# Kernel optimization log

Hardware: AMD Instinct MI355X
Metric: run time of the kernel (lower is better)

Reference implementation:

```python
import jax, jax.numpy as jnp
import numpy as np

B, INPUTS, HIDDEN, OUTPUTS = 128, 512, 512, 512
MAXLEN = INPUTS  # required by the module's bmm/cat shape constraints


def setup_inputs() -> dict:
    key = jax.random.key(0)
    ks = jax.random.split(key, 11)
    s = 0.03
    return {
        "x": jax.random.normal(ks[0], (B, INPUTS, MAXLEN), jnp.float32),
        "attn_W": jax.random.normal(ks[1], (MAXLEN, HIDDEN + INPUTS), jnp.float32) * s,
        "attn_b": jax.random.normal(ks[2], (MAXLEN,), jnp.float32) * s,
        "comb_W": jax.random.normal(ks[3], (HIDDEN, INPUTS + MAXLEN), jnp.float32) * s,
        "comb_b": jax.random.normal(ks[4], (HIDDEN,), jnp.float32) * s,
        "w_ih": jax.random.normal(ks[5], (3 * HIDDEN, HIDDEN), jnp.float32) * s,
        "w_hh": jax.random.normal(ks[6], (3 * HIDDEN, HIDDEN), jnp.float32) * s,
        "b_ih": jax.random.normal(ks[7], (3 * HIDDEN,), jnp.float32) * s,
        "b_hh": jax.random.normal(ks[8], (3 * HIDDEN,), jnp.float32) * s,
        "out_W": jax.random.normal(ks[9], (OUTPUTS, HIDDEN), jnp.float32) * s,
        "out_b": jax.random.normal(ks[10], (OUTPUTS,), jnp.float32) * s,
    }


def reference(x, attn_W, attn_b, comb_W, comb_b, w_ih, w_hh, b_ih, b_hh, out_W, out_b):
    # x: [B, inputs, T] with T == max_length == inputs (shape constraint of the module).
    # The torch code loops over batch with identical per-element math -> vectorize over B,
    # and uses lax.scan over the sequential time dimension.
    Bn = x.shape[0]
    H = w_hh.shape[1]
    xs = jnp.moveaxis(x, 2, 0)  # [T, B, inputs]
    h0 = jnp.zeros((Bn, H), x.dtype)

    def step(h, inp):
        # inp: [B, inputs], h: [B, hidden]
        cat = jnp.concatenate([inp, h], axis=1)                     # [B, inputs+hidden]
        attn_w = jax.nn.softmax(cat @ attn_W.T + attn_b, axis=1)    # [B, max_length]
        applied = jnp.einsum('bm,bmt->bt', attn_w, x)               # [B, T]
        g = jnp.concatenate([inp, applied], axis=1) @ comb_W.T + comb_b
        g = jax.nn.relu(g)                                          # [B, hidden]
        # PyTorch GRU cell
        gi = g @ w_ih.T + b_ih
        gh = h @ w_hh.T + b_hh
        ir, iz, i_n = jnp.split(gi, 3, axis=1)
        hr, hz, h_n = jnp.split(gh, 3, axis=1)
        r = jax.nn.sigmoid(ir + hr)
        z = jax.nn.sigmoid(iz + hz)
        n = jnp.tanh(i_n + r * h_n)
        h_new = (1.0 - z) * n + z * h
        return h_new, None

    h_final, _ = jax.lax.scan(step, h0, xs)
    return h_final @ out_W.T + out_b  # [B, outputs]
```

## Files before the change

kernel.cpp:

```cpp
#include <hip/hip_runtime.h>


typedef unsigned short u16;
typedef unsigned int u32;
typedef _Float16 h2 __attribute__((ext_vector_type(2)));
typedef _Float16 f16x8 __attribute__((ext_vector_type(8)));
typedef float f32x4 __attribute__((ext_vector_type(4)));
typedef float f32x2 __attribute__((ext_vector_type(2)));
typedef u32 u32x4 __attribute__((ext_vector_type(4)));

#define MAGIC 0x13579BDFu

#define OFF_AW   65536
#define OFF_CW   1114112
#define OFF_WIH  2162688
#define OFF_WHH  3735552
#define OFF_OW   5308416
#define OFF_HB   5832704
#define OFF_SF   5963776
#define OFF_AP0  6225920
#define OFF_AP1  6488064
#define OFF_GB   6750208
#define OFF_GH   6881280
#define OFF_XT   7667712
#define WS_NEED  74776576

#define FS_S   64
#define FS_C   96
#define FS_G   128
#define FS_GH  160
#define FS_H   192
#define FS_RDY 224

__device__ __forceinline__ float sigmoidf_(float v) { return 1.f / (1.f + __expf(-v)); }
__device__ __forceinline__ float tanhf_(float v) {
  v = fminf(fmaxf(v, -15.f), 15.f);
  float e2 = __expf(2.f * v);
  return (e2 - 1.f) / (e2 + 1.f);
}
__device__ __forceinline__ u32 packh2(float a, float b) {
  h2 v; v.x = (_Float16)a; v.y = (_Float16)b;
  return __builtin_bit_cast(u32, v);
}

__device__ __forceinline__ void vm_drain() { asm volatile("s_waitcnt vmcnt(0)" ::: "memory"); }

__device__ __forceinline__ f32x2 ldg_f32x2(const void* p) {
  f32x2 r;
  asm volatile("global_load_dwordx2 %0, %1, off sc0 sc1\n\ts_waitcnt vmcnt(0)"
               : "=v"(r) : "v"(p) : "memory");
  return r;
}
__device__ __forceinline__ void ldg4x16(const void* p0, const void* p1, const void* p2,
                                        const void* p3, u32x4& a, u32x4& b, u32x4& c, u32x4& d) {
  asm volatile(
      "global_load_dwordx4 %0, %4, off sc0 sc1\n\t"
      "global_load_dwordx4 %1, %5, off sc0 sc1\n\t"
      "global_load_dwordx4 %2, %6, off sc0 sc1\n\t"
      "global_load_dwordx4 %3, %7, off sc0 sc1\n\t"
      "s_waitcnt vmcnt(0)"
      : "=&v"(a), "=&v"(b), "=&v"(c), "=&v"(d)
      : "v"(p0), "v"(p1), "v"(p2), "v"(p3) : "memory");
}
__device__ __forceinline__ void ldg3_f32(const float* p0, const float* p1, const float* p2,
                                         float& a, float& b, float& c) {
  asm volatile(
      "global_load_dword %0, %3, off sc0 sc1\n\t"
      "global_load_dword %1, %4, off sc0 sc1\n\t"
      "global_load_dword %2, %5, off sc0 sc1\n\t"
      "s_waitcnt vmcnt(0)"
      : "=&v"(a), "=&v"(b), "=&v"(c)
      : "v"(p0), "v"(p1), "v"(p2) : "memory");
}

__device__ __forceinline__ void stg_f32(float* p, float v) {
  asm volatile("global_store_dword %0, %1, off sc0 sc1" :: "v"(p), "v"(v) : "memory");
}
__device__ __forceinline__ void stg_f32x2(float* p, f32x2 v) {
  asm volatile("global_store_dwordx2 %0, %1, off sc0 sc1" :: "v"(p), "v"(v) : "memory");
}
__device__ __forceinline__ void stg_u16(u16* p, u32 v) {
  asm volatile("global_store_short %0, %1, off sc0 sc1" :: "v"(p), "v"(v) : "memory");
}

__device__ __forceinline__ void flag_arrive(u32* ctrl, int fs, int slot, u32 tok) {
  vm_drain();
  __syncthreads();
  if (threadIdx.x == 0) {
    atomicMax(ctrl + fs + slot, tok);
  }
}
__device__ __forceinline__ void flag_wait(u32* ctrl, int fs, int n, u32 tok, int lane) {
  if (tok == 0u) return;
  u32* p = ctrl + fs;
  for (;;) {
    u32 v = tok;
    if (lane < n) v = __hip_atomic_load(p + lane, __ATOMIC_RELAXED, __HIP_MEMORY_SCOPE_AGENT);
    if (__all((int)(v >= tok))) break;
  }
}

__device__ __forceinline__ void stage_rows(const u16* gsrc, char* lds, int tid) {
  const int row = tid >> 4, c = tid & 15;
  const u16* g = gsrc + row * 512 + c * 32;
  u32x4 a, b, cc, d;
  ldg4x16(g, g + 8, g + 16, g + 24, a, b, cc, d);
  u32x4* dst = (u32x4*)(lds + row * 1040 + c * 64);
  dst[0] = a; dst[1] = b; dst[2] = cc; dst[3] = d;
}

#define MFMA(a, b, c) __builtin_amdgcn_mfma_f32_16x16x32_f16((a), (b), (c), 0, 0, 0)

extern "C" __global__ void __launch_bounds__(256, 1)
rnn_fused(const float* __restrict__ x, const float* __restrict__ attn_W,
          const float* __restrict__ attn_b, const float* __restrict__ comb_W,
          const float* __restrict__ comb_b, const float* __restrict__ w_ih,
          const float* __restrict__ w_hh, const float* __restrict__ b_ih,
          const float* __restrict__ b_hh, const float* __restrict__ out_W,
          const float* __restrict__ out_b, float* __restrict__ out,
          char* __restrict__ ws)
{
  const int tid  = threadIdx.x;
  const int lane = tid & 63;
  const int warp = tid >> 6;
  const int team = blockIdx.x & 7;
  const int tb   = blockIdx.x >> 3;
  const int tt   = tb * 256 + tid;
  const int gb0  = team * 16;
  const int lb   = tb >> 1;
  const int half = tb & 1;
  const int b    = gb0 + lb;
  const int m0h  = half * 256;

  u32* ctrl = (u32*)ws + team * 1024;

  u16*   AW  = (u16*)(ws + OFF_AW);
  u16*   CW  = (u16*)(ws + OFF_CW);
  u16*   WIH = (u16*)(ws + OFF_WIH);
  u16*   WHH = (u16*)(ws + OFF_WHH);
  u16*   OW  = (u16*)(ws + OFF_OW);
  u16*   HB  = (u16*)(ws + OFF_HB);
  float* Sf  = (float*)(ws + OFF_SF);
  float* AP0 = (float*)(ws + OFF_AP0);
  float* AP1 = (float*)(ws + OFF_AP1);
  u16*   GB  = (u16*)(ws + OFF_GB);
  float* GH  = (float*)(ws + OFF_GH);
  u16*   XT  = (u16*)(ws + OFF_XT);

  __shared__ char smem[16704];
  float*     tbuf   = (float*)smem;
  u32*       pLDS   = (u32*)smem;
  float*     redbuf = (float*)(smem + 512);
  float*     rbuf   = (float*)(smem + 8704);
  _Float16*  ldsF   = (_Float16*)smem;

  if (tb == 0) {
    for (int i = 1 + tid; i < 1024; i += 256) ctrl[i] = 0u;
    __syncthreads();
    if (tid == 0) { __threadfence(); atomicExch(ctrl, MAGIC); }
  }
  if (tid == 0) {
    while (__hip_atomic_load(ctrl, __ATOMIC_RELAXED, __HIP_MEMORY_SCOPE_AGENT) != MAGIC) {}
    __threadfence();
  }
  __syncthreads();

  for (int i = tt; i < 512 * 1024; i += 8192) AW[i]  = __builtin_bit_cast(u16, (_Float16)attn_W[i]);
  for (int i = tt; i < 512 * 1024; i += 8192) CW[i]  = __builtin_bit_cast(u16, (_Float16)comb_W[i]);
  for (int i = tt; i < 1536 * 512; i += 8192) WIH[i] = __builtin_bit_cast(u16, (_Float16)w_ih[i]);
  for (int i = tt; i < 1536 * 512; i += 8192) WHH[i] = __builtin_bit_cast(u16, (_Float16)w_hh[i]);
  for (int i = tt; i < 512 * 512;  i += 8192) OW[i]  = __builtin_bit_cast(u16, (_Float16)out_W[i]);
  HB[(size_t)gb0 * 512 + tt] = 0;

  {
    const float* xb  = x  + (size_t)b * 512 * 512;
    u16*         xtB = XT + (size_t)b * 512 * 512;
    for (int mt = 0; mt < 4; ++mt) {
      for (int ct = 0; ct < 8; ++ct) {
        for (int rr = warp; rr < 64; rr += 4)
          tbuf[rr * 65 + lane] = xb[(size_t)(m0h + mt * 64 + rr) * 512 + ct * 64 + lane];
        __syncthreads();
        for (int rr = warp; rr < 64; rr += 4)
          xtB[(size_t)(ct * 64 + rr) * 512 + m0h + mt * 64 + lane] =
              __builtin_bit_cast(u16, (_Float16)tbuf[lane * 65 + rr]);
        __syncthreads();
      }
    }
  }

  vm_drain();
  __syncthreads();
  if (tid == 0) { __threadfence(); atomicMax(ctrl + FS_RDY + tb, 1u); }
  {
    u32* p = ctrl + FS_RDY;
    for (;;) {
      u32 v = 1u;
      if (lane < 32) v = __hip_atomic_load(p + lane, __ATOMIC_RELAXED, __HIP_MEMORY_SCOPE_AGENT);
      if (__all((int)(v >= 1u))) break;
    }
  }
  __syncthreads();
  __threadfence();

  uint4 xr4[64];
  {
    const u16* base = XT + (size_t)b * 262144 + m0h + warp * 64;
#pragma unroll
    for (int r = 0; r < 8; ++r) {
      const uint4* row = (const uint4*)(base + (size_t)(lane * 8 + r) * 512);
#pragma unroll
      for (int jj = 0; jj < 8; ++jj) xr4[r * 8 + jj] = row[jj];
    }
  }

  const int  r16 = lane & 15, q = lane >> 4, q8 = q * 8;
  const bool isA = (tb < 8), isW = (tb >= 8 && tb < 16);
  const int  W4 = ((tb < 8) ? tb : tb - 8) * 4 + warp;
  const int  n0 = W4 * 16;

  float biasA = 0.f, biasD = 0.f, biasI0 = 0.f, biasI1 = 0.f, biasI2 = 0.f,
        biasH0 = 0.f, biasH1 = 0.f, biasH2 = 0.f, biasO = 0.f;
  if (isA) {
    biasA = attn_b[n0 + r16]; biasD = comb_b[n0 + r16];
    biasI0 = b_ih[n0 + r16]; biasI1 = b_ih[512 + n0 + r16]; biasI2 = b_ih[1024 + n0 + r16];
    biasO = out_b[n0 + r16];
  }
  if (isW) {
    biasH0 = b_hh[n0 + r16]; biasH1 = b_hh[512 + n0 + r16]; biasH2 = b_hh[1024 + n0 + r16];
  }

  float hreg[4] = {0.f, 0.f, 0.f, 0.f};

  for (int t = 0; t < 512; ++t) {
    const u32 tok = (u32)(t + 1);

    if (isA) {
      flag_wait(ctrl, FS_H, 8, (u32)t, lane);
      __syncthreads();
      stage_rows(HB + gb0 * 512, smem, tid);
      __syncthreads();
      f32x4 acc = {0.f, 0.f, 0.f, 0.f};
      const u16* aXp = XT + (size_t)(gb0 + r16) * 262144 + (size_t)t * 512 + q8;
      const _Float16* aHl = ldsF + r16 * 520 + q8;
      const u16* bWp = AW + (size_t)(n0 + r16) * 1024 + q8;
#pragma unroll 4
      for (int k0 = 0; k0 < 512; k0 += 32)
        acc = MFMA(*(const f16x8*)(aXp + k0), *(const f16x8*)(bWp + k0), acc);
#pragma unroll 4
      for (int k0 = 0; k0 < 512; k0 += 32)
        acc = MFMA(*(const f16x8*)(aHl + k0), *(const f16x8*)(bWp + 512 + k0), acc);
#pragma unroll
      for (int i = 0; i < 4; ++i)
        stg_f32(Sf + (size_t)(gb0 + q * 4 + i) * 512 + n0 + r16, acc[i] + biasA);
      flag_arrive(ctrl, FS_S, tb, tok);
    } else if (isW) {
      flag_wait(ctrl, FS_H, 8, (u32)t, lane);
      __syncthreads();
      stage_rows(HB + gb0 * 512, smem, tid);
      __syncthreads();
      f32x4 a0 = {0.f,0.f,0.f,0.f}, a1 = {0.f,0.f,0.f,0.f}, a2 = {0.f,0.f,0.f,0.f};
      const _Float16* aHl = ldsF + r16 * 520 + q8;
      const u16* b0p = WHH + (size_t)(n0 + r16) * 512 + q8;
      const u16* b1p = WHH + (size_t)(512 + n0 + r16) * 512 + q8;
      const u16* b2p = WHH + (size_t)(1024 + n0 + r16) * 512 + q8;
#pragma unroll 4
      for (int k0 = 0; k0 < 512; k0 += 32) {
        f16x8 a = *(const f16x8*)(aHl + k0);
        a0 = MFMA(a, *(const f16x8*)(b0p + k0), a0);
        a1 = MFMA(a, *(const f16x8*)(b1p + k0), a1);
        a2 = MFMA(a, *(const f16x8*)(b2p + k0), a2);
      }
#pragma unroll
      for (int i = 0; i < 4; ++i) {
        const size_t ro = (size_t)(gb0 + q * 4 + i) * 1536;
        stg_f32(GH + ro + n0 + r16,        a0[i] + biasH0);
        stg_f32(GH + ro + 512 + n0 + r16,  a1[i] + biasH1);
        stg_f32(GH + ro + 1024 + n0 + r16, a2[i] + biasH2);
      }
      flag_arrive(ctrl, FS_GH, tb - 8, tok);
    }

    flag_wait(ctrl, FS_S, 8, tok, lane);
    {
      const int tc = 2 * tid;
      f32x2 sv = ldg_f32x2(Sf + (size_t)b * 512 + tc);
      float s0 = sv.x, s1 = sv.y;
      float mx = fmaxf(s0, s1);
#pragma unroll
      for (int off = 32; off; off >>= 1) mx = fmaxf(mx, __shfl_xor(mx, off, 64));
      if (lane == 0) rbuf[warp] = mx;
      __syncthreads();
      mx = fmaxf(fmaxf(rbuf[0], rbuf[1]), fmaxf(rbuf[2], rbuf[3]));
      float e0 = __expf(s0 - mx), e1 = __expf(s1 - mx);
      float sm = e0 + e1;
#pragma unroll
      for (int off = 32; off; off >>= 1) sm += __shfl_xor(sm, off, 64);
      if (lane == 0) rbuf[4 + warp] = sm;
      __syncthreads();
      sm = rbuf[4] + rbuf[5] + rbuf[6] + rbuf[7];
      const float inv = 1.f / sm;
      if ((tid >> 7) == half) {
        pLDS[tid & 127] = packh2(e0 * inv, e1 * inv);
      }
      __syncthreads();

      uint4 pz4[8];
      const uint4* pp = (const uint4*)pLDS + warp * 8;
#pragma unroll
      for (int jj = 0; jj < 8; ++jj) pz4[jj] = pp[jj];
      float accr[8];
#pragma unroll
      for (int r = 0; r < 8; ++r) {
        h2 sA = {(_Float16)0.f, (_Float16)0.f};
        h2 sB = {(_Float16)0.f, (_Float16)0.f};
#pragma unroll
        for (int jj = 0; jj < 8; ++jj) {
          uint4 xw = xr4[r * 8 + jj], pw = pz4[jj];
          sA = __builtin_bit_cast(h2, xw.x) * __builtin_bit_cast(h2, pw.x) + sA;
          sB = __builtin_bit_cast(h2, xw.y) * __builtin_bit_cast(h2, pw.y) + sB;
          sA = __builtin_bit_cast(h2, xw.z) * __builtin_bit_cast(h2, pw.z) + sA;
          sB = __builtin_bit_cast(h2, xw.w) * __builtin_bit_cast(h2, pw.w) + sB;
        }
        accr[r] = (float)sA.x + (float)sA.y + (float)sB.x + (float)sB.y;
      }
#pragma unroll
      for (int r = 0; r < 8; ++r) redbuf[warp * 512 + lane * 8 + r] = accr[r];
      __syncthreads();
      {
        float v0 = redbuf[tc]     + redbuf[512 + tc]     + redbuf[1024 + tc]     + redbuf[1536 + tc];
        float v1 = redbuf[tc + 1] + redbuf[512 + tc + 1] + redbuf[1024 + tc + 1] + redbuf[1536 + tc + 1];
        float* dst = (half ? AP1 : AP0) + (size_t)b * 512 + tc;
        f32x2 vv; vv.x = v0; vv.y = v1;
        stg_f32x2(dst, vv);
      }
      flag_arrive(ctrl, FS_C, tb, tok);
    }

    if (isA) {
      f32x4 acc = {0.f, 0.f, 0.f, 0.f};
      const u16* aXp = XT + (size_t)(gb0 + r16) * 262144 + (size_t)t * 512 + q8;
      const u16* bWp = CW + (size_t)(n0 + r16) * 1024 + q8;
#pragma unroll 4
      for (int k0 = 0; k0 < 512; k0 += 32)
        acc = MFMA(*(const f16x8*)(aXp + k0), *(const f16x8*)(bWp + k0), acc);
      flag_wait(ctrl, FS_C, 32, tok, lane);
      __syncthreads();
      {
        const int row = tid >> 4, c = tid & 15;
        const float* g0 = AP0 + (size_t)(gb0 + row) * 512 + c * 32;
        const float* g1 = AP1 + (size_t)(gb0 + row) * 512 + c * 32;
        u32* dst = (u32*)(smem + row * 1040 + c * 64);
        u32x4 A0, A1, A2, A3, B0, B1, B2, B3, C0, C1, C2, C3, D0, D1, D2, D3;
        ldg4x16(g0,      g0 + 4,  g0 + 8,  g0 + 12, A0, A1, A2, A3);
        ldg4x16(g0 + 16, g0 + 20, g0 + 24, g0 + 28, B0, B1, B2, B3);
        ldg4x16(g1,      g1 + 4,  g1 + 8,  g1 + 12, C0, C1, C2, C3);
        ldg4x16(g1 + 16, g1 + 20, g1 + 24, g1 + 28, D0, D1, D2, D3);
        f32x4 s0 = __builtin_bit_cast(f32x4, A0) + __builtin_bit_cast(f32x4, C0);
        f32x4 s1 = __builtin_bit_cast(f32x4, A1) + __builtin_bit_cast(f32x4, C1);
        f32x4 s2 = __builtin_bit_cast(f32x4, A2) + __builtin_bit_cast(f32x4, C2);
        f32x4 s3 = __builtin_bit_cast(f32x4, A3) + __builtin_bit_cast(f32x4, C3);
        f32x4 s4 = __builtin_bit_cast(f32x4, B0) + __builtin_bit_cast(f32x4, D0);
        f32x4 s5 = __builtin_bit_cast(f32x4, B1) + __builtin_bit_cast(f32x4, D1);
        f32x4 s6 = __builtin_bit_cast(f32x4, B2) + __builtin_bit_cast(f32x4, D2);
        f32x4 s7 = __builtin_bit_cast(f32x4, B3) + __builtin_bit_cast(f32x4, D3);
        dst[0]  = packh2(s0[0], s0[1]); dst[1]  = packh2(s0[2], s0[3]);
        dst[2]  = packh2(s1[0], s1[1]); dst[3]  = packh2(s1[2], s1[3]);
        dst[4]  = packh2(s2[0], s2[1]); dst[5]  = packh2(s2[2], s2[3]);
        dst[6]  = packh2(s3[0], s3[1]); dst[7]  = packh2(s3[2], s3[3]);
        dst[8]  = packh2(s4[0], s4[1]); dst[9]  = packh2(s4[2], s4[3]);
        dst[10] = packh2(s5[0], s5[1]); dst[11] = packh2(s5[2], s5[3]);
        dst[12] = packh2(s6[0], s6[1]); dst[13] = packh2(s6[2], s6[3]);
        dst[14] = packh2(s7[0], s7[1]); dst[15] = packh2(s7[2], s7[3]);
      }
      __syncthreads();
      const _Float16* aAl = ldsF + r16 * 520 + q8;
#pragma unroll 4
      for (int k0 = 0; k0 < 512; k0 += 32)
        acc = MFMA(*(const f16x8*)(aAl + k0), *(const f16x8*)(bWp + 512 + k0), acc);
#pragma unroll
      for (int i = 0; i < 4; ++i) {
        float g = fmaxf(acc[i] + biasD, 0.f);
        stg_u16(GB + (size_t)(gb0 + q * 4 + i) * 512 + n0 + r16,
                (u32)__builtin_bit_cast(u16, (_Float16)g));
      }
      flag_arrive(ctrl, FS_G, tb, tok);
      flag_wait(ctrl, FS_G, 8, tok, lane);
      __syncthreads();
      stage_rows(GB + gb0 * 512, smem, tid);
      __syncthreads();

      f32x4 g0 = {0.f,0.f,0.f,0.f}, g1 = {0.f,0.f,0.f,0.f}, g2 = {0.f,0.f,0.f,0.f};
      const _Float16* aGl = ldsF + r16 * 520 + q8;
      const u16* w0p = WIH + (size_t)(n0 + r16) * 512 + q8;
      const u16* w1p = WIH + (size_t)(512 + n0 + r16) * 512 + q8;
      const u16* w2p = WIH + (size_t)(1024 + n0 + r16) * 512 + q8;
#pragma unroll 4
      for (int k0 = 0; k0 < 512; k0 += 32) {
        f16x8 a = *(const f16x8*)(aGl + k0);
        g0 = MFMA(a, *(const f16x8*)(w0p + k0), g0);
        g1 = MFMA(a, *(const f16x8*)(w1p + k0), g1);
        g2 = MFMA(a, *(const f16x8*)(w2p + k0), g2);
      }
      flag_wait(ctrl, FS_GH, 8, tok, lane);
#pragma unroll
      for (int i = 0; i < 4; ++i) {
        const int bi = gb0 + q * 4 + i;
        const size_t ro = (size_t)bi * 1536;
        const int j = n0 + r16;
        float ghr_, ghz_, ghn_;
        ldg3_f32(GH + ro + j, GH + ro + 512 + j, GH + ro + 1024 + j, ghr_, ghz_, ghn_);
        float gir = g0[i] + biasI0, giz = g1[i] + biasI1, gin = g2[i] + biasI2;
        float rg = sigmoidf_(gir + ghr_);
        float zg = sigmoidf_(giz + ghz_);
        float ng = tanhf_(gin + rg * ghn_);
        hreg[i] = (1.f - zg) * ng + zg * hreg[i];
        stg_u16(HB + (size_t)bi * 512 + j,
                (u32)__builtin_bit_cast(u16, (_Float16)hreg[i]));
      }
      flag_arrive(ctrl, FS_H, tb, tok);
    }
  }

  if (isA) {
    flag_wait(ctrl, FS_H, 8, 512u, lane);
    __syncthreads();
    stage_rows(HB + gb0 * 512, smem, tid);
    __syncthreads();
    f32x4 acc = {0.f, 0.f, 0.f, 0.f};
    const _Float16* aHl = ldsF + r16 * 520 + q8;
    const u16* bOp = OW + (size_t)(n0 + r16) * 512 + q8;
#pragma unroll 4
    for (int k0 = 0; k0 < 512; k0 += 32)
      acc = MFMA(*(const f16x8*)(aHl + k0), *(const f16x8*)(bOp + k0), acc);
#pragma unroll
    for (int i = 0; i < 4; ++i)
      out[(size_t)(gb0 + q * 4 + i) * 512 + n0 + r16] = acc[i] + biasO;
  }
}

extern "C" void kernel_launch(void* const* d_in, const int* in_sizes, int n_in,
                              void* d_out, int out_size, void* d_ws, size_t ws_size,
                              hipStream_t stream) {
  if (ws_size < (size_t)WS_NEED) return;
  rnn_fused<<<dim3(256), dim3(256), 0, stream>>>(
      (const float*)d_in[0], (const float*)d_in[1], (const float*)d_in[2],
      (const float*)d_in[3], (const float*)d_in[4], (const float*)d_in[5],
      (const float*)d_in[6], (const float*)d_in[7], (const float*)d_in[8],
      (const float*)d_in[9], (const float*)d_in[10],
      (float*)d_out, (char*)d_ws);
}
```

Baseline: 20.89 ms.

## Replace per-block max flags with shared atomic counters and batch global loads

Inter-block synchronisation switches from one atomicMax slot per block, polled by several lanes with a wave vote, to one atomicAdd counter per stage that only warp 0 polls before a block barrier. Global loads are batched: staged rows use immediate offsets from one base pointer, the AP0/AP1 reduction issues all sixteen loads with a single wait, and the twelve GH loads for the four batch rows share one wait instead of four. The intent is to cut polling traffic and latency on the serial per-timestep critical path. Counters now grow monotonically, so correctness depends on the control area being zeroed before each launch, and all blocks contend on one atomic address.

Result: faster. 20.12 ms (-3.7%).

```diff
diff --git a/kernel.cpp b/kernel.cpp
--- a/kernel.cpp
+++ b/kernel.cpp
@@ -51,26 +51,63 @@
                : "=v"(r) : "v"(p) : "memory");
   return r;
 }
-__device__ __forceinline__ void ldg4x16(const void* p0, const void* p1, const void* p2,
-                                        const void* p3, u32x4& a, u32x4& b, u32x4& c, u32x4& d) {
+__device__ __forceinline__ void ldg4x16_off(const void* p, u32x4& a, u32x4& b, u32x4& c, u32x4& d) {
   asm volatile(
       "global_load_dwordx4 %0, %4, off sc0 sc1\n\t"
-      "global_load_dwordx4 %1, %5, off sc0 sc1\n\t"
-      "global_load_dwordx4 %2, %6, off sc0 sc1\n\t"
-      "global_load_dwordx4 %3, %7, off sc0 sc1\n\t"
+      "global_load_dwordx4 %1, %4, off offset:16 sc0 sc1\n\t"
+      "global_load_dwordx4 %2, %4, off offset:32 sc0 sc1\n\t"
+      "global_load_dwordx4 %3, %4, off offset:48 sc0 sc1\n\t"
       "s_waitcnt vmcnt(0)"
       : "=&v"(a), "=&v"(b), "=&v"(c), "=&v"(d)
-      : "v"(p0), "v"(p1), "v"(p2), "v"(p3) : "memory");
-}
-__device__ __forceinline__ void ldg3_f32(const float* p0, const float* p1, const float* p2,
-                                         float& a, float& b, float& c) {
+      : "v"(p) : "memory");
+}
+__device__ __forceinline__ void ldg_ap16(const float* pa, const float* pb,
+                                         u32x4 (&A)[8], u32x4 (&B)[8]) {
   asm volatile(
-      "global_load_dword %0, %3, off sc0 sc1\n\t"
-      "global_load_dword %1, %4, off sc0 sc1\n\t"
-      "global_load_dword %2, %5, off sc0 sc1\n\t"
+      "global_load_dwordx4 %0, %16, off sc0 sc1\n\t"
+      "global_load_dwordx4 %1, %16, off offset:16 sc0 sc1\n\t"
+      "global_load_dwordx4 %2, %16, off offset:32 sc0 sc1\n\t"
+      "global_load_dwordx4 %3, %16, off offset:48 sc0 sc1\n\t"
+      "global_load_dwordx4 %4, %16, off offset:64 sc0 sc1\n\t"
+      "global_load_dwordx4 %5, %16, off offset:80 sc0 sc1\n\t"
+      "global_load_dwordx4 %6, %16, off offset:96 sc0 sc1\n\t"
+      "global_load_dwordx4 %7, %16, off offset:112 sc0 sc1\n\t"
+      "global_load_dwordx4 %8, %17, off sc0 sc1\n\t"
+      "global_load_dwordx4 %9, %17, off offset:16 sc0 sc1\n\t"
+      "global_load_dwordx4 %10, %17, off offset:32 sc0 sc1\n\t"
+      "global_load_dwordx4 %11, %17, off offset:48 sc0 sc1\n\t"
+      "global_load_dwordx4 %12, %17, off offset:64 sc0 sc1\n\t"
+      "global_load_dwordx4 %13, %17, off offset:80 sc0 sc1\n\t"
+      "global_load_dwordx4 %14, %17, off offset:96 sc0 sc1\n\t"
+      "global_load_dwordx4 %15, %17, off offset:112 sc0 sc1\n\t"
       "s_waitcnt vmcnt(0)"
-      : "=&v"(a), "=&v"(b), "=&v"(c)
-      : "v"(p0), "v"(p1), "v"(p2) : "memory");
+      : "=&v"(A[0]), "=&v"(A[1]), "=&v"(A[2]), "=&v"(A[3]),
+        "=&v"(A[4]), "=&v"(A[5]), "=&v"(A[6]), "=&v"(A[7]),
+        "=&v"(B[0]), "=&v"(B[1]), "=&v"(B[2]), "=&v"(B[3]),
+        "=&v"(B[4]), "=&v"(B[5]), "=&v"(B[6]), "=&v"(B[7])
+      : "v"(pa), "v"(pb) : "memory");
+}
+__device__ __forceinline__ void ldg_gh12(const float* q0, const float* q1,
+                                         const float* q2, const float* q3,
+                                         float (&rr)[4], float (&zz)[4], float (&nn)[4]) {
+  asm volatile(
+      "global_load_dword %0, %12, off offset:-2048 sc0 sc1\n\t"
+      "global_load_dword %4, %12, off sc0 sc1\n\t"
+      "global_load_dword %8, %12, off offset:2048 sc0 sc1\n\t"
+      "global_load_dword %1, %13, off offset:-2048 sc0 sc1\n\t"
+      "global_load_dword %5, %13, off sc0 sc1\n\t"
+      "global_load_dword %9, %13, off offset:2048 sc0 sc1\n\t"
+      "global_load_dword %2, %14, off offset:-2048 sc0 sc1\n\t"
+      "global_load_dword %6, %14, off sc0 sc1\n\t"
+      "global_load_dword %10, %14, off offset:2048 sc0 sc1\n\t"
+      "global_load_dword %3, %15, off offset:-2048 sc0 sc1\n\t"
+      "global_load_dword %7, %15, off sc0 sc1\n\t"
+      "global_load_dword %11, %15, off offset:2048 sc0 sc1\n\t"
+      "s_waitcnt vmcnt(0)"
+      : "=&v"(rr[0]), "=&v"(rr[1]), "=&v"(rr[2]), "=&v"(rr[3]),
+        "=&v"(zz[0]), "=&v"(zz[1]), "=&v"(zz[2]), "=&v"(zz[3]),
+        "=&v"(nn[0]), "=&v"(nn[1]), "=&v"(nn[2]), "=&v"(nn[3])
+      : "v"(q0), "v"(q1), "v"(q2), "v"(q3) : "memory");
 }
 
 __device__ __forceinline__ void stg_f32(float* p, float v) {
@@ -83,28 +120,26 @@
   asm volatile("global_store_short %0, %1, off sc0 sc1" :: "v"(p), "v"(v) : "memory");
 }
 
-__device__ __forceinline__ void flag_arrive(u32* ctrl, int fs, int slot, u32 tok) {
+__device__ __forceinline__ void flag_add(u32* ctrl, int fs) {
   vm_drain();
   __syncthreads();
-  if (threadIdx.x == 0) {
-    atomicMax(ctrl + fs + slot, tok);
-  }
-}
-__device__ __forceinline__ void flag_wait(u32* ctrl, int fs, int n, u32 tok, int lane) {
-  if (tok == 0u) return;
-  u32* p = ctrl + fs;
-  for (;;) {
-    u32 v = tok;
-    if (lane < n) v = __hip_atomic_load(p + lane, __ATOMIC_RELAXED, __HIP_MEMORY_SCOPE_AGENT);
-    if (__all((int)(v >= tok))) break;
-  }
+  if (threadIdx.x == 0) atomicAdd(ctrl + fs, 1u);
+}
+__device__ __forceinline__ void flag_wait_ge(u32* ctrl, int fs, u32 target, int warp) {
+  if (warp == 0) {
+    u32 v;
+    do {
+      v = __hip_atomic_load(ctrl + fs, __ATOMIC_RELAXED, __HIP_MEMORY_SCOPE_AGENT);
+    } while (v < target);
+  }
+  __syncthreads();
 }
 
 __device__ __forceinline__ void stage_rows(const u16* gsrc, char* lds, int tid) {
   const int row = tid >> 4, c = tid & 15;
   const u16* g = gsrc + row * 512 + c * 32;
   u32x4 a, b, cc, d;
-  ldg4x16(g, g + 8, g + 16, g + 24, a, b, cc, d);
+  ldg4x16_off(g, a, b, cc, d);
   u32x4* dst = (u32x4*)(lds + row * 1040 + c * 64);
   dst[0] = a; dst[1] = b; dst[2] = cc; dst[3] = d;
 }
@@ -190,16 +225,8 @@
 
   vm_drain();
   __syncthreads();
-  if (tid == 0) { __threadfence(); atomicMax(ctrl + FS_RDY + tb, 1u); }
-  {
-    u32* p = ctrl + FS_RDY;
-    for (;;) {
-      u32 v = 1u;
-      if (lane < 32) v = __hip_atomic_load(p + lane, __ATOMIC_RELAXED, __HIP_MEMORY_SCOPE_AGENT);
-      if (__all((int)(v >= 1u))) break;
-    }
-  }
-  __syncthreads();
+  if (tid == 0) { __threadfence(); atomicAdd(ctrl + FS_RDY, 1u); }
+  flag_wait_ge(ctrl, FS_RDY, 32u, warp);
   __threadfence();
 
   uint4 xr4[64];
@@ -235,8 +262,7 @@
     const u32 tok = (u32)(t + 1);
 
     if (isA) {
-      flag_wait(ctrl, FS_H, 8, (u32)t, lane);
-      __syncthreads();
+      flag_wait_ge(ctrl, FS_H, 8u * (u32)t, warp);
       stage_rows(HB + gb0 * 512, smem, tid);
       __syncthreads();
       f32x4 acc = {0.f, 0.f, 0.f, 0.f};
@@ -252,10 +278,9 @@
 #pragma unroll
       for (int i = 0; i < 4; ++i)
         stg_f32(Sf + (size_t)(gb0 + q * 4 + i) * 512 + n0 + r16, acc[i] + biasA);
-      flag_arrive(ctrl, FS_S, tb, tok);
+      flag_add(ctrl, FS_S);
     } else if (isW) {
-      flag_wait(ctrl, FS_H, 8, (u32)t, lane);
-      __syncthreads();
+      flag_wait_ge(ctrl, FS_H, 8u * (u32)t, warp);
       stage_rows(HB + gb0 * 512, smem, tid);
       __syncthreads();
       f32x4 a0 = {0.f,0.f,0.f,0.f}, a1 = {0.f,0.f,0.f,0.f}, a2 = {0.f,0.f,0.f,0.f};
@@ -277,10 +302,10 @@
         stg_f32(GH + ro + 512 + n0 + r16,  a1[i] + biasH1);
         stg_f32(GH + ro + 1024 + n0 + r16, a2[i] + biasH2);
       }
-      flag_arrive(ctrl, FS_GH, tb - 8, tok);
+      flag_add(ctrl, FS_GH);
     }
 
-    flag_wait(ctrl, FS_S, 8, tok, lane);
+    flag_wait_ge(ctrl, FS_S, 8u * tok, warp);
     {
       const int tc = 2 * tid;
       f32x2 sv = ldg_f32x2(Sf + (size_t)b * 512 + tc);
@@ -333,7 +358,7 @@
         f32x2 vv; vv.x = v0; vv.y = v1;
         stg_f32x2(dst, vv);
       }
-      flag_arrive(ctrl, FS_C, tb, tok);
+      flag_add(ctrl, FS_C);
     }
 
     if (isA) {
@@ -343,34 +368,20 @@
 #pragma unroll 4
       for (int k0 = 0; k0 < 512; k0 += 32)
         acc = MFMA(*(const f16x8*)(aXp + k0), *(const f16x8*)(bWp + k0), acc);
-      flag_wait(ctrl, FS_C, 32, tok, lane);
-      __syncthreads();
+      flag_wait_ge(ctrl, FS_C, 32u * tok, warp);
       {
         const int row = tid >> 4, c = tid & 15;
         const float* g0 = AP0 + (size_t)(gb0 + row) * 512 + c * 32;
         const float* g1 = AP1 + (size_t)(gb0 + row) * 512 + c * 32;
         u32* dst = (u32*)(smem + row * 1040 + c * 64);
-        u32x4 A0, A1, A2, A3, B0, B1, B2, B3, C0, C1, C2, C3, D0, D1, D2, D3;
-        ldg4x16(g0,      g0 + 4,  g0 + 8,  g0 + 12, A0, A1, A2, A3);
-        ldg4x16(g0 + 16, g0 + 20, g0 + 24, g0 + 28, B0, B1, B2, B3);
-        ldg4x16(g1,      g1 + 4,  g1 + 8,  g1 + 12, C0, C1, C2, C3);
-        ldg4x16(g1 + 16, g1 + 20, g1 + 24, g1 + 28, D0, D1, D2, D3);
-        f32x4 s0 = __builtin_bit_cast(f32x4, A0) + __builtin_bit_cast(f32x4, C0);
-        f32x4 s1 = __builtin_bit_cast(f32x4, A1) + __builtin_bit_cast(f32x4, C1);
-        f32x4 s2 = __builtin_bit_cast(f32x4, A2) + __builtin_bit_cast(f32x4, C2);
-        f32x4 s3 = __builtin_bit_cast(f32x4, A3) + __builtin_bit_cast(f32x4, C3);
-        f32x4 s4 = __builtin_bit_cast(f32x4, B0) + __builtin_bit_cast(f32x4, D0);
-        f32x4 s5 = __builtin_bit_cast(f32x4, B1) + __builtin_bit_cast(f32x4, D1);
-        f32x4 s6 = __builtin_bit_cast(f32x4, B2) + __builtin_bit_cast(f32x4, D2);
-        f32x4 s7 = __builtin_bit_cast(f32x4, B3) + __builtin_bit_cast(f32x4, D3);
-        dst[0]  = packh2(s0[0], s0[1]); dst[1]  = packh2(s0[2], s0[3]);
-        dst[2]  = packh2(s1[0], s1[1]); dst[3]  = packh2(s1[2], s1[3]);
-        dst[4]  = packh2(s2[0], s2[1]); dst[5]  = packh2(s2[2], s2[3]);
-        dst[6]  = packh2(s3[0], s3[1]); dst[7]  = packh2(s3[2], s3[3]);
-        dst[8]  = packh2(s4[0], s4[1]); dst[9]  = packh2(s4[2], s4[3]);
-        dst[10] = packh2(s5[0], s5[1]); dst[11] = packh2(s5[2], s5[3]);
-        dst[12] = packh2(s6[0], s6[1]); dst[13] = packh2(s6[2], s6[3]);
-        dst[14] = packh2(s7[0], s7[1]); dst[15] = packh2(s7[2], s7[3]);
+        u32x4 A[8], B[8];
+        ldg_ap16(g0, g1, A, B);
+#pragma unroll
+        for (int k = 0; k < 8; ++k) {
+          f32x4 s = __builtin_bit_cast(f32x4, A[k]) + __builtin_bit_cast(f32x4, B[k]);
+          dst[2 * k]     = packh2(s[0], s[1]);
+          dst[2 * k + 1] = packh2(s[2], s[3]);
+        }
       }
       __syncthreads();
       const _Float16* aAl = ldsF + r16 * 520 + q8;
@@ -383,9 +394,8 @@
         stg_u16(GB + (size_t)(gb0 + q * 4 + i) * 512 + n0 + r16,
                 (u32)__builtin_bit_cast(u16, (_Float16)g));
       }
-      flag_arrive(ctrl, FS_G, tb, tok);
-      flag_wait(ctrl, FS_G, 8, tok, lane);
-      __syncthreads();
+      flag_add(ctrl, FS_G);
+      flag_wait_ge(ctrl, FS_G, 8u * tok, warp);
       stage_rows(GB + gb0 * 512, smem, tid);
       __syncthreads();
 
@@ -401,29 +411,33 @@
         g1 = MFMA(a, *(const f16x8*)(w1p + k0), g1);
         g2 = MFMA(a, *(const f16x8*)(w2p + k0), g2);
       }
-      flag_wait(ctrl, FS_GH, 8, tok, lane);
-#pragma unroll
-      for (int i = 0; i < 4; ++i) {
-        const int bi = gb0 + q * 4 + i;
-        const size_t ro = (size_t)bi * 1536;
+      flag_wait_ge(ctrl, FS_GH, 8u * tok, warp);
+      {
         const int j = n0 + r16;
-        float ghr_, ghz_, ghn_;
-        ldg3_f32(GH + ro + j, GH + ro + 512 + j, GH + ro + 1024 + j, ghr_, ghz_, ghn_);
-        float gir = g0[i] + biasI0, giz = g1[i] + biasI1, gin = g2[i] + biasI2;
-        float rg = sigmoidf_(gir + ghr_);
-        float zg = sigmoidf_(giz + ghz_);
-        float ng = tanhf_(gin + rg * ghn_);
-        hreg[i] = (1.f - zg) * ng + zg * hreg[i];
-        stg_u16(HB + (size_t)bi * 512 + j,
-                (u32)__builtin_bit_cast(u16, (_Float16)hreg[i]));
-      }
-      flag_arrive(ctrl, FS_H, tb, tok);
+        const float* q0p = GH + (size_t)(gb0 + q * 4 + 0) * 1536 + 512 + j;
+        const float* q1p = GH + (size_t)(gb0 + q * 4 + 1) * 1536 + 512 + j;
+        const float* q2p = GH + (size_t)(gb0 + q * 4 + 2) * 1536 + 512 + j;
+        const float* q3p = GH + (size_t)(gb0 + q * 4 + 3) * 1536 + 512 + j;
+        float ghr[4], ghz[4], ghn[4];
+        ldg_gh12(q0p, q1p, q2p, q3p, ghr, ghz, ghn);
+#pragma unroll
+        for (int i = 0; i < 4; ++i) {
+          const int bi = gb0 + q * 4 + i;
+          float gir = g0[i] + biasI0, giz = g1[i] + biasI1, gin = g2[i] + biasI2;
+          float rg = sigmoidf_(gir + ghr[i]);
+          float zg = sigmoidf_(giz + ghz[i]);
+          float ng = tanhf_(gin + rg * ghn[i]);
+          hreg[i] = (1.f - zg) * ng + zg * hreg[i];
+          stg_u16(HB + (size_t)bi * 512 + j,
+                  (u32)__builtin_bit_cast(u16, (_Float16)hreg[i]));
+        }
+      }
+      flag_add(ctrl, FS_H);
     }
   }
 
   if (isA) {
-    flag_wait(ctrl, FS_H, 8, 512u, lane);
-    __syncthreads();
+    flag_wait_ge(ctrl, FS_H, 8u * 512u, warp);
     stage_rows(HB + gb0 * 512, smem, tid);
     __syncthreads();
     f32x4 acc = {0.f, 0.f, 0.f, 0.f};
```
